# Kernel tuning notes

Measured on AMD Instinct MI355X. Metric: run time of the kernel, lower is better.

## Reference

```python
import jax, jax.numpy as jnp
import numpy as np

EPS = 1e-5
K = 5


def _bn(h, g, b):
    # BatchNorm1d in training mode: batch stats over all dims except channels.
    ax = tuple(range(h.ndim - 1))
    mu = jnp.mean(h, axis=ax, keepdims=True)
    var = jnp.var(h, axis=ax, keepdims=True)
    return g * (h - mu) * jax.lax.rsqrt(var + EPS) + b


def _block(x, w, b, g, be):
    # Lin -> ReLU -> BN, as in MLP() helper
    return _bn(jax.nn.relu(x @ w + b), g, be)


def _knn_idx(x, k):
    # x: [B, P, D]; k nearest per point (includes self at distance 0)
    sq = jnp.sum(x * x, axis=-1)
    d2 = sq[:, :, None] + sq[:, None, :] - 2.0 * jnp.einsum('bpd,bqd->bpq', x, x)
    return jax.lax.top_k(-d2, k)[1]  # [B, P, k]


def _edge_conv(x, k, mlp_fn):
    # DynamicEdgeConv: recompute kNN graph on current features, gather
    # neighbor/center pairs, per-edge MLP on [x_i, x_j - x_i], max-aggregate.
    idx = _knn_idx(x, k)                                   # [B,P,k]
    xj = jax.vmap(lambda xb, ib: xb[ib])(x, idx)           # [B,P,k,D]
    xi = jnp.broadcast_to(x[:, :, None, :], xj.shape)
    e = jnp.concatenate([xi, xj - xi], axis=-1)            # [B,P,k,2D]
    return jnp.max(mlp_fn(e), axis=2)                      # max aggr -> [B,P,C]


def dec_forward(pos,
                c1w0, c1b0, c1g0, c1e0,
                c1w1, c1b1, c1g1, c1e1,
                c1w2, c1b2, c1g2, c1e2,
                c2w, c2b, c2g, c2e,
                l1w, l1b, l1g, l1e,
                m1w, m1b, m1g, m1e,
                m2w, m2b, m2g, m2e,
                m3w, m3b):
    mlp1 = lambda e: _block(_block(_block(e, c1w0, c1b0, c1g0, c1e0),
                                   c1w1, c1b1, c1g1, c1e1),
                            c1w2, c1b2, c1g2, c1e2)
    x1 = _edge_conv(pos, K, mlp1)                          # [B,P,64]
    x2 = _edge_conv(x1, K, lambda e: _block(e, c2w, c2b, c2g, c2e))  # [B,P,128]
    h = _block(jnp.concatenate([x1, x2], axis=-1), l1w, l1b, l1g, l1e)  # [B,P,1024]
    p = jnp.max(h, axis=1)                                 # global_max_pool -> [B,1024]
    p = _block(p, m1w, m1b, m1g, m1e)                      # dropout omitted (eval)
    p = _block(p, m2w, m2b, m2g, m2e)
    return p @ m3w + m3b                                   # [B, n_classes]


def setup_inputs() -> dict:
    key = jax.random.key(0)
    ks = jax.random.split(key, 12)
    B, P = 16, 2048

    def w(k, shape):
        return 0.05 * jax.random.normal(k, shape, jnp.float32)

    z = lambda c: jnp.zeros((c,), jnp.float32)
    o = lambda c: jnp.ones((c,), jnp.float32)

    d = {
        'pos': jax.random.normal(ks[0], (B, P, 3), jnp.float32),
        'c1w0': w(ks[1], (6, 64)), 'c1b0': z(64), 'c1g0': o(64), 'c1e0': z(64),
        'c1w1': w(ks[2], (64, 64)), 'c1b1': z(64), 'c1g1': o(64), 'c1e1': z(64),
        'c1w2': w(ks[3], (64, 64)), 'c1b2': z(64), 'c1g2': o(64), 'c1e2': z(64),
        'c2w': w(ks[4], (128, 128)), 'c2b': z(128), 'c2g': o(128), 'c2e': z(128),
        'l1w': w(ks[5], (192, 1024)), 'l1b': z(1024), 'l1g': o(1024), 'l1e': z(1024),
        'm1w': w(ks[6], (1024, 512)), 'm1b': z(512), 'm1g': o(512), 'm1e': z(512),
        'm2w': w(ks[7], (512, 256)), 'm2b': z(256), 'm2g': o(256), 'm2e': z(256),
        'm3w': w(ks[8], (256, 2)), 'm3b': z(2),
    }
    return d


def reference(pos,
              c1w0, c1b0, c1g0, c1e0,
              c1w1, c1b1, c1g1, c1e1,
              c1w2, c1b2, c1g2, c1e2,
              c2w, c2b, c2g, c2e,
              l1w, l1b, l1g, l1e,
              m1w, m1b, m1g, m1e,
              m2w, m2b, m2g, m2e,
              m3w, m3b):
    return dec_forward(pos,
                       c1w0, c1b0, c1g0, c1e0,
                       c1w1, c1b1, c1g1, c1e1,
                       c1w2, c1b2, c1g2, c1e2,
                       c2w, c2b, c2g, c2e,
                       l1w, l1b, l1g, l1e,
                       m1w, m1b, m1g, m1e,
                       m2w, m2b, m2g, m2e,
                       m3w, m3b)
```

## Files before the change

### kernel.cpp

```cpp
#include <hip/hip_runtime.h>
#include <cmath>

constexpr int B = 16, P = 2048, KNN = 5;
constexpr int BP = B * P;
constexpr int E = BP * KNN;
constexpr float EPS = 1e-5f;
constexpr int QC2 = 2;

constexpr int ST0 = 0;
constexpr int ST1 = 128;
constexpr int ST2 = 256;
constexpr int ST3 = 384;
constexpr int ST4 = 640;
constexpr int ST5 = 2688;
constexpr int ST6 = 3712;
constexpr int ST_TOTAL = 4224;

typedef __attribute__((ext_vector_type(8))) short bf16x8;
typedef __attribute__((ext_vector_type(4))) float f32x4;

__device__ inline unsigned short f2bf(float x) {
    unsigned u = __float_as_uint(x);
    unsigned r = (u + 0x7FFFu + ((u >> 16) & 1u)) >> 16;
    return (unsigned short)r;
}
__device__ inline float bf2f(unsigned short h) {
    return __uint_as_float(((unsigned)h) << 16);
}
__device__ inline void split2bf(float x, unsigned short& h, unsigned short& l) {
    unsigned short hh = f2bf(x);
    h = hh;
    l = f2bf(x - bf2f(hh));
}

__device__ inline void ins5(float d, int qi, float bd[KNN], int bi[KNN]) {
    bool c0 = d < bd[0], c1 = d < bd[1], c2 = d < bd[2], c3 = d < bd[3], c4 = d < bd[4];
    bd[4] = c3 ? bd[3] : (c4 ? d : bd[4]);  bi[4] = c3 ? bi[3] : (c4 ? qi : bi[4]);
    bd[3] = c2 ? bd[2] : (c3 ? d : bd[3]);  bi[3] = c2 ? bi[2] : (c3 ? qi : bi[3]);
    bd[2] = c1 ? bd[1] : (c2 ? d : bd[2]);  bi[2] = c1 ? bi[1] : (c2 ? qi : bi[2]);
    bd[1] = c0 ? bd[0] : (c1 ? d : bd[1]);  bi[1] = c0 ? bi[0] : (c1 ? qi : bi[1]);
    bd[0] = c0 ? d : bd[0];                 bi[0] = c0 ? qi : bi[0];
}
__device__ inline void ins5t(float d, int qi, float bd[KNN], int bi[KNN]) {
    bool c0 = (d < bd[0]) || (d == bd[0] && qi < bi[0]);
    bool c1 = (d < bd[1]) || (d == bd[1] && qi < bi[1]);
    bool c2 = (d < bd[2]) || (d == bd[2] && qi < bi[2]);
    bool c3 = (d < bd[3]) || (d == bd[3] && qi < bi[3]);
    bool c4 = (d < bd[4]) || (d == bd[4] && qi < bi[4]);
    bd[4] = c3 ? bd[3] : (c4 ? d : bd[4]);  bi[4] = c3 ? bi[3] : (c4 ? qi : bi[4]);
    bd[3] = c2 ? bd[2] : (c3 ? d : bd[3]);  bi[3] = c2 ? bi[2] : (c3 ? qi : bi[3]);
    bd[2] = c1 ? bd[1] : (c2 ? d : bd[2]);  bi[2] = c1 ? bi[1] : (c2 ? qi : bi[2]);
    bd[1] = c0 ? bd[0] : (c1 ? d : bd[1]);  bi[1] = c0 ? bi[0] : (c1 ? qi : bi[1]);
    bd[0] = c0 ? d : bd[0];                 bi[0] = c0 ? qi : bi[0];
}

__global__ void k_init(float* __restrict__ stats, float* __restrict__ pmax,
                       float* __restrict__ pmin) {
    int i = blockIdx.x * 256 + threadIdx.x;
    if (i < ST_TOTAL) stats[i] = 0.f;
    if (i < B * 1024) { pmax[i] = 0.f; pmin[i] = INFINITY; }
}

__global__ __launch_bounds__(256) void k_redstat(const float* __restrict__ part,
        float* __restrict__ stats, int nblk) {
    __shared__ float r[256];
    int slot = blockIdx.x;
    float s = 0.f;
    for (int i = threadIdx.x; i < nblk; i += 256)
        s += part[(size_t)i * 128 + slot];
    r[threadIdx.x] = s; __syncthreads();
    for (int o = 128; o; o >>= 1) {
        if (threadIdx.x < o) r[threadIdx.x] += r[threadIdx.x + o];
        __syncthreads();
    }
    if (threadIdx.x == 0) stats[slot] = r[0];
}

__global__ void k_wsplit(const float* __restrict__ w, unsigned short* __restrict__ th,
                         unsigned short* __restrict__ tl, int K, int N) {
    int i = blockIdx.x * 256 + threadIdx.x;
    if (i >= K * N) return;
    int k = i / N, n = i - k * N;
    float f = w[i];
    unsigned short h = f2bf(f);
    th[(size_t)n * K + k] = h;
    tl[(size_t)n * K + k] = f2bf(f - bf2f(h));
}

__global__ __launch_bounds__(64) void k_wfold(const float* __restrict__ stats,
        const float* __restrict__ g, const float* __restrict__ be,
        const float* __restrict__ w, const float* __restrict__ bias,
        unsigned short* __restrict__ wfh, unsigned short* __restrict__ wfl,
        float* __restrict__ bias2, float invN) {
    __shared__ float red[64];
    int n = blockIdx.x, k = threadIdx.x;
    float mu = stats[k] * invN;
    float var = stats[64 + k] * invN - mu * mu;
    float sc = g[k] * rsqrtf(var + EPS);
    float sh = be[k] - mu * sc;
    float wv = w[k * 64 + n];
    float wf = sc * wv;
    unsigned short h, l;
    split2bf(wf, h, l);
    wfh[n * 64 + k] = h; wfl[n * 64 + k] = l;
    red[k] = sh * wv; __syncthreads();
    for (int o = 32; o; o >>= 1) {
        if (k < o) red[k] += red[k + o];
        __syncthreads();
    }
    if (k == 0) bias2[n] = bias[n] + red[0];
}

__global__ void k_wprep2(const float* __restrict__ w,
        unsigned short* __restrict__ wdh, unsigned short* __restrict__ wdl,
        unsigned short* __restrict__ w1h, unsigned short* __restrict__ w1l) {
    int i = blockIdx.x * 256 + threadIdx.x;
    if (i >= 64 * 128) return;
    int k = i >> 7, n = i & 127;
    float w0 = w[k * 128 + n];
    float w1 = w[(64 + k) * 128 + n];
    float wd = w0 - w1;
    unsigned short h, l;
    split2bf(wd, h, l); wdh[n * 64 + k] = h; wdl[n * 64 + k] = l;
    split2bf(w1, h, l); w1h[n * 64 + k] = h; w1l[n * 64 + k] = l;
}

__global__ void k_xsplit(const float* __restrict__ x, unsigned short* __restrict__ xh,
                         unsigned short* __restrict__ xl) {
    int i = blockIdx.x * 256 + threadIdx.x;
    float f = x[i];
    unsigned short h, l;
    split2bf(f, h, l);
    xh[i] = h; xl[i] = l;
}

__global__ __launch_bounds__(256) void k_knn1(const float* __restrict__ pos,
                                              int* __restrict__ idx1) {
    __shared__ float4 qt[2048];
    int b = blockIdx.x >> 5;
    int p0 = (blockIdx.x & 31) << 6;
    const float* posb = pos + (size_t)b * P * 3;
#pragma unroll
    for (int t = 0; t < 8; ++t) {
        int q = (t << 8) + threadIdx.x;
        float qx = posb[q * 3 + 0], qy = posb[q * 3 + 1], qz = posb[q * 3 + 2];
        qt[q] = make_float4(qx, qy, qz, qx * qx + qy * qy + qz * qz);
    }
    __syncthreads();
    int pl = threadIdx.x >> 2, sub = threadIdx.x & 3;
    int p = p0 + pl;
    float4 me = qt[p];
    float x = me.x, y = me.y, z = me.z, sqp = me.w;
    float bd[KNN]; int bi[KNN];
#pragma unroll
    for (int i = 0; i < KNN; ++i) { bd[i] = INFINITY; bi[i] = 0; }
    for (int j0 = 0; j0 < 512; j0 += 8) {
        float4 v[8];
#pragma unroll
        for (int u = 0; u < 8; ++u) v[u] = qt[((j0 + u) << 2) | sub];
#pragma unroll
        for (int u = 0; u < 8; ++u) {
            float dot = x * v[u].x + y * v[u].y + z * v[u].z;
            float d2 = sqp + v[u].w - 2.f * dot;
            if (d2 < bd[KNN - 1]) ins5(d2, ((j0 + u) << 2) | sub, bd, bi);
        }
    }
#pragma unroll
    for (int w = 1; w <= 2; w <<= 1) {
        float od[KNN]; int oi[KNN];
#pragma unroll
        for (int i = 0; i < KNN; ++i) {
            od[i] = __shfl_xor(bd[i], w, 64);
            oi[i] = __shfl_xor(bi[i], w, 64);
        }
#pragma unroll
        for (int i = 0; i < KNN; ++i) ins5t(od[i], oi[i], bd, bi);
    }
    if (sub == 0) {
        size_t o = ((size_t)b * P + p) * KNN;
#pragma unroll
        for (int i = 0; i < KNN; ++i) idx1[o + i] = bi[i];
    }
}

__global__ __launch_bounds__(256) void k_ec1_l0(const float* __restrict__ pos,
        const int* __restrict__ idx1, const float* __restrict__ w,
        const float* __restrict__ bias, unsigned short* __restrict__ zh,
        unsigned short* __restrict__ zl, float* __restrict__ part) {
    __shared__ float elds[256][6];
    __shared__ float red[256];
    int tid = threadIdx.x;
    int base = blockIdx.x * 256;
    {
        int e = base + tid;
        int bp = e / KNN;
        int bb = bp >> 11;
        int q = idx1[e];
        const float* pi = pos + (size_t)bp * 3;
        const float* pj = pos + ((size_t)(bb << 11) + q) * 3;
        float x0 = pi[0], x1v = pi[1], x2v = pi[2];
        elds[tid][0] = x0; elds[tid][1] = x1v; elds[tid][2] = x2v;
        elds[tid][3] = pj[0] - x0; elds[tid][4] = pj[1] - x1v; elds[tid][5] = pj[2] - x2v;
    }
    int c = tid & 63, lane = tid >> 6;
    float wr[6];
#pragma unroll
    for (int d = 0; d < 6; ++d) wr[d] = w[d * 64 + c];
    float bc = bias[c];
    __syncthreads();
    float s1 = 0.f, s2 = 0.f;
    for (int i = 0; i < 64; ++i) {
        int e = lane + (i << 2);
        float acc = bc;
#pragma unroll
        for (int d = 0; d < 6; ++d) acc = fmaf(elds[e][d], wr[d], acc);
        acc = fmaxf(acc, 0.f);
        unsigned short h, l;
        split2bf(acc, h, l);
        zh[(size_t)(base + e) * 64 + c] = h;
        zl[(size_t)(base + e) * 64 + c] = l;
        s1 += acc; s2 = fmaf(acc, acc, s2);
    }
    red[tid] = s1; __syncthreads();
    if (tid < 64) part[(size_t)blockIdx.x * 128 + tid] =
        red[tid] + red[tid + 64] + red[tid + 128] + red[tid + 192];
    __syncthreads();
    red[tid] = s2; __syncthreads();
    if (tid < 64) part[(size_t)blockIdx.x * 128 + 64 + tid] =
        red[tid] + red[tid + 64] + red[tid + 128] + red[tid + 192];
}

__global__ __launch_bounds__(128) void k_lin64m(
        const unsigned short* __restrict__ zinh, const unsigned short* __restrict__ zinl,
        const unsigned short* __restrict__ wfh, const unsigned short* __restrict__ wfl,
        const float* __restrict__ bias2, unsigned short* __restrict__ zouth,
        unsigned short* __restrict__ zoutl, float* __restrict__ part) {
    __shared__ float red[2 * 64 * 2];
    int tid = threadIdx.x;
    int wv = tid >> 6, lane = tid & 63;
    int l15 = lane & 15, quad = lane >> 4;
    int row0 = blockIdx.x * 128 + wv * 64;
    f32x4 acc[4][4];
#pragma unroll
    for (int i = 0; i < 4; ++i)
#pragma unroll
        for (int j = 0; j < 4; ++j) acc[i][j] = (f32x4)0.f;

#pragma unroll
    for (int kc = 0; kc < 2; ++kc) {
        bf16x8 afh[4], afl[4], bfh[4], bfl[4];
#pragma unroll
        for (int i = 0; i < 4; ++i) {
            size_t o = (size_t)(row0 + i * 16 + l15) * 64 + kc * 32 + quad * 8;
            afh[i] = *(const bf16x8*)&zinh[o];
            afl[i] = *(const bf16x8*)&zinl[o];
        }
#pragma unroll
        for (int j = 0; j < 4; ++j) {
            size_t wo = (size_t)(j * 16 + l15) * 64 + kc * 32 + quad * 8;
            bfh[j] = *(const bf16x8*)&wfh[wo];
            bfl[j] = *(const bf16x8*)&wfl[wo];
        }
#pragma unroll
        for (int i = 0; i < 4; ++i)
#pragma unroll
            for (int j = 0; j < 4; ++j) {
                acc[i][j] = __builtin_amdgcn_mfma_f32_16x16x32_bf16(afh[i], bfh[j], acc[i][j], 0, 0, 0);
                acc[i][j] = __builtin_amdgcn_mfma_f32_16x16x32_bf16(afh[i], bfl[j], acc[i][j], 0, 0, 0);
                acc[i][j] = __builtin_amdgcn_mfma_f32_16x16x32_bf16(afl[i], bfh[j], acc[i][j], 0, 0, 0);
            }
    }
#pragma unroll
    for (int j = 0; j < 4; ++j) {
        int colL = j * 16 + l15;
        float bl = bias2[colL];
        float s1 = 0.f, s2 = 0.f;
#pragma unroll
        for (int i = 0; i < 4; ++i) {
            int row = row0 + i * 16 + quad * 4;
#pragma unroll
            for (int r = 0; r < 4; ++r) {
                float v = fmaxf(acc[i][j][r] + bl, 0.f);
                unsigned short h, l;
                split2bf(v, h, l);
                zouth[(size_t)(row + r) * 64 + colL] = h;
                zoutl[(size_t)(row + r) * 64 + colL] = l;
                s1 += v; s2 = fmaf(v, v, s2);
            }
        }
        s1 += __shfl_xor(s1, 16, 64); s1 += __shfl_xor(s1, 32, 64);
        s2 += __shfl_xor(s2, 16, 64); s2 += __shfl_xor(s2, 32, 64);
        if (quad == 0) {
            red[(wv * 64 + colL) * 2 + 0] = s1;
            red[(wv * 64 + colL) * 2 + 1] = s2;
        }
    }
    __syncthreads();
    if (tid < 64) {
        part[(size_t)blockIdx.x * 128 + tid] =
            red[tid * 2] + red[(64 + tid) * 2];
        part[(size_t)blockIdx.x * 128 + 64 + tid] =
            red[tid * 2 + 1] + red[(64 + tid) * 2 + 1];
    }
}

__global__ __launch_bounds__(256) void k_ec1_fin(const unsigned short* __restrict__ z2h,
        const unsigned short* __restrict__ z2l,
        const float* __restrict__ statsIn, const float* __restrict__ g,
        const float* __restrict__ be, float* __restrict__ x1,
        float* __restrict__ sq2) {
    int tid = threadIdx.x;
    int o = blockIdx.x * 256 + tid;
    int c = o & 63; int bp = o >> 6;
    float mu = statsIn[c] * (1.f / E);
    float var = statsIn[64 + c] * (1.f / E) - mu * mu;
    float sc = g[c] * rsqrtf(var + EPS);
    float sh = be[c] - mu * sc;
    float m = -INFINITY;
#pragma unroll
    for (int j = 0; j < KNN; ++j) {
        size_t zo = ((size_t)bp * KNN + j) * 64 + c;
        float v = bf2f(z2h[zo]) + bf2f(z2l[zo]);
        m = fmaxf(m, fmaf(v, sc, sh));
    }
    x1[o] = m;
    float ss = m * m;
#pragma unroll
    for (int off = 32; off; off >>= 1) ss += __shfl_down(ss, off, 64);
    if (c == 0) sq2[bp] = ss;
}

__global__ __launch_bounds__(128, 1) void k_knn2(const unsigned short* __restrict__ x1h,
        const unsigned short* __restrict__ x1l, const float* __restrict__ sq2,
        float* __restrict__ cd, int* __restrict__ ci) {
    __shared__ float S[2][32 * 129];
    int tid = threadIdx.x;
    int wv = tid >> 6, lane = tid & 63;
    int l15 = lane & 15, quad = lane >> 4;
    int qc = blockIdx.x & (QC2 - 1);
    int pt = blockIdx.x >> 1;
    int b = pt >> 5;
    int pw = ((pt & 31) << 6) + wv * 32;
    const size_t xbase = (size_t)b * P * 64;
    float* Sw = &S[wv][0];

    bf16x8 ah[2][2], al[2][2];
#pragma unroll
    for (int i = 0; i < 2; ++i)
#pragma unroll
        for (int kc = 0; kc < 2; ++kc) {
            size_t o = xbase + (size_t)(pw + i * 16 + l15) * 64 + kc * 32 + quad * 8;
            ah[i][kc] = *(const bf16x8*)&x1h[o];
            al[i][kc] = *(const bf16x8*)&x1l[o];
        }

    int half = lane >> 5;
    int pidx = lane & 31;
    float bd[KNN]; int bi[KNN];
#pragma unroll
    for (int i = 0; i < KNN; ++i) { bd[i] = INFINITY; bi[i] = 0; }

    int qlo = qc << 10;
    for (int t = 0; t < 8; ++t) {
        int q0 = qlo + (t << 7);
        float qsv[8];
#pragma unroll
        for (int j = 0; j < 8; ++j) qsv[j] = sq2[b * P + q0 + j * 16 + l15];
        f32x4 acc[2][8];
#pragma unroll
        for (int i = 0; i < 2; ++i)
#pragma unroll
            for (int j = 0; j < 8; ++j) acc[i][j] = (f32x4)0.f;
#pragma unroll
        for (int kc = 0; kc < 2; ++kc) {
            bf16x8 bh[8], bl[8];
#pragma unroll
            for (int j = 0; j < 8; ++j) {
                size_t o = xbase + (size_t)(q0 + j * 16 + l15) * 64 + kc * 32 + quad * 8;
                bh[j] = *(const bf16x8*)&x1h[o];
                bl[j] = *(const bf16x8*)&x1l[o];
            }
#pragma unroll
            for (int i = 0; i < 2; ++i)
#pragma unroll
                for (int j = 0; j < 8; ++j) {
                    acc[i][j] = __builtin_amdgcn_mfma_f32_16x16x32_bf16(ah[i][kc], bh[j], acc[i][j], 0, 0, 0);
                    acc[i][j] = __builtin_amdgcn_mfma_f32_16x16x32_bf16(ah[i][kc], bl[j], acc[i][j], 0, 0, 0);
                    acc[i][j] = __builtin_amdgcn_mfma_f32_16x16x32_bf16(al[i][kc], bh[j], acc[i][j], 0, 0, 0);
                }
        }
#pragma unroll
        for (int i = 0; i < 2; ++i)
#pragma unroll
            for (int j = 0; j < 8; ++j)
#pragma unroll
                for (int r = 0; r < 4; ++r) {
                    int pl = i * 16 + quad * 4 + r;
                    Sw[pl * 129 + j * 16 + l15] = fmaf(acc[i][j][r], -2.f, qsv[j]);
                }
        const float* row = Sw + pidx * 129 + half * 64;
        int qb = q0 + half * 64;
        for (int jj = 0; jj < 64; jj += 4) {
            float k0 = row[jj + 0], k1 = row[jj + 1], k2 = row[jj + 2], k3 = row[jj + 3];
            if (k0 < bd[4]) ins5(k0, qb + jj + 0, bd, bi);
            if (k1 < bd[4]) ins5(k1, qb + jj + 1, bd, bi);
            if (k2 < bd[4]) ins5(k2, qb + jj + 2, bd, bi);
            if (k3 < bd[4]) ins5(k3, qb + jj + 3, bd, bi);
        }
    }
#pragma unroll
    for (int i = 0; i < KNN; ++i) {
        float od = __shfl_xor(bd[i], 32, 64);
        int oi = __shfl_xor(bi[i], 32, 64);
        if (half == 0) ins5t(od, oi, bd, bi);
    }
    if (half == 0) {
        size_t o = (((size_t)b * P + pw + pidx) * QC2 + qc) * KNN;
#pragma unroll
        for (int i = 0; i < KNN; ++i) { cd[o + i] = bd[i]; ci[o + i] = bi[i]; }
    }
}

__global__ __launch_bounds__(256) void k_knn2m(const float* __restrict__ cd,
        const int* __restrict__ ci, int* __restrict__ idx2) {
    int bp = blockIdx.x * 256 + threadIdx.x;
    float bd[KNN]; int bi[KNN];
#pragma unroll
    for (int i = 0; i < KNN; ++i) { bd[i] = INFINITY; bi[i] = 0; }
    size_t o = (size_t)bp * QC2 * KNN;
    for (int t = 0; t < QC2 * KNN; ++t) {
        float d2 = cd[o + t]; int qi = ci[o + t];
        if (d2 < bd[KNN - 1]) ins5(d2, qi, bd, bi);
    }
#pragma unroll
    for (int i = 0; i < KNN; ++i) idx2[bp * KNN + i] = bi[i];
}

__global__ __launch_bounds__(256) void k_ec2m(
        const unsigned short* __restrict__ x1h, const unsigned short* __restrict__ x1l,
        const int* __restrict__ idx2,
        const unsigned short* __restrict__ wdh, const unsigned short* __restrict__ wdl,
        const unsigned short* __restrict__ w1h, const unsigned short* __restrict__ w1l,
        const float* __restrict__ bias, float* __restrict__ zout,
        float* __restrict__ stats) {
    __shared__ float red[2 * 128 * 2];
    int tid = threadIdx.x;
    int base = blockIdx.x * 128;
    int bb = base / (P * KNN);
    int wv = tid >> 6, lane = tid & 63;
    int wm = wv >> 1, wn = wv & 1;
    int l15 = lane & 15, quad = lane >> 4;
    int rI[4], rJ[4];
#pragma unroll
    for (int i = 0; i < 4; ++i) {
        int e = base + wm * 64 + i * 16 + l15;
        rI[i] = e / KNN;
        rJ[i] = (bb << 11) + idx2[e];
    }
    f32x4 acc[4][4];
#pragma unroll
    for (int i = 0; i < 4; ++i)
#pragma unroll
        for (int j = 0; j < 4; ++j) acc[i][j] = (f32x4)0.f;

#pragma unroll
    for (int s = 0; s < 2; ++s) {
        const unsigned short* bh_ = s ? w1h : wdh;
        const unsigned short* bl_ = s ? w1l : wdl;
#pragma unroll
        for (int kc = 0; kc < 2; ++kc) {
            bf16x8 afh[4], afl[4], bfh[4], bfl[4];
#pragma unroll
            for (int i = 0; i < 4; ++i) {
                int row = s ? rJ[i] : rI[i];
                size_t o = (size_t)row * 64 + kc * 32 + quad * 8;
                afh[i] = *(const bf16x8*)&x1h[o];
                afl[i] = *(const bf16x8*)&x1l[o];
            }
#pragma unroll
            for (int j = 0; j < 4; ++j) {
                size_t wo = (size_t)(wn * 64 + j * 16 + l15) * 64 + kc * 32 + quad * 8;
                bfh[j] = *(const bf16x8*)&bh_[wo];
                bfl[j] = *(const bf16x8*)&bl_[wo];
            }
#pragma unroll
            for (int i = 0; i < 4; ++i)
#pragma unroll
                for (int j = 0; j < 4; ++j) {
                    acc[i][j] = __builtin_amdgcn_mfma_f32_16x16x32_bf16(afh[i], bfh[j], acc[i][j], 0, 0, 0);
                    acc[i][j] = __builtin_amdgcn_mfma_f32_16x16x32_bf16(afh[i], bfl[j], acc[i][j], 0, 0, 0);
                    acc[i][j] = __builtin_amdgcn_mfma_f32_16x16x32_bf16(afl[i], bfh[j], acc[i][j], 0, 0, 0);
                }
        }
    }
#pragma unroll
    for (int j = 0; j < 4; ++j) {
        int colL = wn * 64 + j * 16 + l15;
        float bl = bias[colL];
        float s1 = 0.f, s2 = 0.f;
#pragma unroll
        for (int i = 0; i < 4; ++i) {
            int row = wm * 64 + i * 16 + quad * 4;
#pragma unroll
            for (int r = 0; r < 4; ++r) {
                float v = fmaxf(acc[i][j][r] + bl, 0.f);
                zout[(size_t)(base + row + r) * 128 + colL] = v;
                s1 += v; s2 = fmaf(v, v, s2);
            }
        }
        s1 += __shfl_xor(s1, 16, 64); s1 += __shfl_xor(s1, 32, 64);
        s2 += __shfl_xor(s2, 16, 64); s2 += __shfl_xor(s2, 32, 64);
        if (quad == 0) {
            red[(wm * 128 + colL) * 2 + 0] = s1;
            red[(wm * 128 + colL) * 2 + 1] = s2;
        }
    }
    __syncthreads();
    if (tid < 128) {
        atomicAdd(&stats[tid], red[tid * 2] + red[(128 + tid) * 2]);
        atomicAdd(&stats[128 + tid], red[tid * 2 + 1] + red[(128 + tid) * 2 + 1]);
    }
}

__global__ __launch_bounds__(256) void k_ec2_fin(const float* __restrict__ z3,
        const float* __restrict__ stats, const float* __restrict__ g,
        const float* __restrict__ be, float* __restrict__ x2) {
    int o = blockIdx.x * 256 + threadIdx.x;
    int c = o & 127; int bp = o >> 7;
    float mu = stats[c] * (1.f / E);
    float var = stats[128 + c] * (1.f / E) - mu * mu;
    float sc = g[c] * rsqrtf(var + EPS);
    float sh = be[c] - mu * sc;
    float m = -INFINITY;
#pragma unroll
    for (int j = 0; j < KNN; ++j)
        m = fmaxf(m, fmaf(z3[((size_t)bp * KNN + j) * 128 + c], sc, sh));
    x2[o] = m;
}

__device__ __forceinline__ void gl16(unsigned short* lds, const unsigned short* g) {
    __builtin_amdgcn_global_load_lds(
        (const __attribute__((address_space(1))) unsigned int*)g,
        (__attribute__((address_space(3))) unsigned int*)lds, 16, 0, 0);
}

__global__ __launch_bounds__(256) void k_l1m(
        const unsigned short* __restrict__ x1h, const unsigned short* __restrict__ x1l,
        const unsigned short* __restrict__ x2h, const unsigned short* __restrict__ x2l,
        const unsigned short* __restrict__ wth, const unsigned short* __restrict__ wtl,
        const float* __restrict__ bias, float* __restrict__ stats,
        float* __restrict__ pmax, float* __restrict__ pmin) {
    __shared__ unsigned short Ah[128 * 32], Al[128 * 32];
    __shared__ unsigned short Bh[128 * 32], Bl[128 * 32];
    __shared__ float red[2 * 128 * 4];
    int tid = threadIdx.x;
    int brow = blockIdx.x & 255;
    int bcol = blockIdx.x >> 8;
    int row0 = brow << 7, col0 = bcol << 7;
    int wv = tid >> 6, lane = tid & 63;
    int wm = wv >> 1, wn = wv & 1;
    int l15 = lane & 15, quad = lane >> 4;
    int rloc = wv * 16 + (lane >> 2);
    int ch8 = (lane & 3) * 8;
    f32x4 acc[4][4];
#pragma unroll
    for (int i = 0; i < 4; ++i)
#pragma unroll
        for (int j = 0; j < 4; ++j) acc[i][j] = (f32x4)0.f;

#pragma unroll
    for (int t = 0; t < 6; ++t) {
        int k0 = t * 32;
        const unsigned short* ah = (k0 < 64) ? x1h : x2h;
        const unsigned short* al = (k0 < 64) ? x1l : x2l;
        int astr = (k0 < 64) ? 64 : 128;
        int aoff = (k0 < 64) ? k0 : (k0 - 64);
#pragma unroll
        for (int c = 0; c < 2; ++c) {
            int rl = c * 64 + rloc;
            size_t ao = (size_t)(row0 + rl) * astr + aoff + ch8;
            size_t bo = (size_t)(col0 + rl) * 192 + k0 + ch8;
            int lb = (c * 64 + wv * 16) * 32;
            gl16(&Ah[lb], &ah[ao]);
            gl16(&Al[lb], &al[ao]);
            gl16(&Bh[lb], &wth[bo]);
            gl16(&Bl[lb], &wtl[bo]);
        }
        __syncthreads();
        bf16x8 afh[4], afl[4], bfh[4], bfl[4];
#pragma unroll
        for (int i = 0; i < 4; ++i) {
            int o = (wm * 64 + i * 16 + l15) * 32 + quad * 8;
            afh[i] = *(const bf16x8*)&Ah[o];
            afl[i] = *(const bf16x8*)&Al[o];
        }
#pragma unroll
        for (int j = 0; j < 4; ++j) {
            int o = (wn * 64 + j * 16 + l15) * 32 + quad * 8;
            bfh[j] = *(const bf16x8*)&Bh[o];
            bfl[j] = *(const bf16x8*)&Bl[o];
        }
#pragma unroll
        for (int i = 0; i < 4; ++i)
#pragma unroll
            for (int j = 0; j < 4; ++j) {
                acc[i][j] = __builtin_amdgcn_mfma_f32_16x16x32_bf16(afh[i], bfh[j], acc[i][j], 0, 0, 0);
                acc[i][j] = __builtin_amdgcn_mfma_f32_16x16x32_bf16(afh[i], bfl[j], acc[i][j], 0, 0, 0);
                acc[i][j] = __builtin_amdgcn_mfma_f32_16x16x32_bf16(afl[i], bfh[j], acc[i][j], 0, 0, 0);
            }
        __syncthreads();
    }
#pragma unroll
    for (int j = 0; j < 4; ++j) {
        int colL = wn * 64 + j * 16 + l15;
        float bl = bias[col0 + colL];
        float s1 = 0.f, s2 = 0.f, mx = 0.f, mn = INFINITY;
#pragma unroll
        for (int i = 0; i < 4; ++i)
#pragma unroll
            for (int r = 0; r < 4; ++r) {
                float v = fmaxf(acc[i][j][r] + bl, 0.f);
                s1 += v; s2 = fmaf(v, v, s2);
                mx = fmaxf(mx, v); mn = fminf(mn, v);
            }
        s1 += __shfl_xor(s1, 16, 64); s1 += __shfl_xor(s1, 32, 64);
        s2 += __shfl_xor(s2, 16, 64); s2 += __shfl_xor(s2, 32, 64);
        mx = fmaxf(mx, __shfl_xor(mx, 16, 64)); mx = fmaxf(mx, __shfl_xor(mx, 32, 64));
        mn = fminf(mn, __shfl_xor(mn, 16, 64)); mn = fminf(mn, __shfl_xor(mn, 32, 64));
        if (quad == 0) {
            float* rp = &red[(wm * 128 + colL) * 4];
            rp[0] = s1; rp[1] = s2; rp[2] = mx; rp[3] = mn;
        }
    }
    __syncthreads();
    if (tid < 128) {
        const float* r0 = &red[tid * 4];
        const float* r1 = &red[(128 + tid) * 4];
        int bb = row0 >> 11;
        atomicAdd(&stats[col0 + tid], r0[0] + r1[0]);
        atomicAdd(&stats[1024 + col0 + tid], r0[1] + r1[1]);
        atomicMax((unsigned int*)&pmax[bb * 1024 + col0 + tid],
                  __float_as_uint(fmaxf(r0[2], r1[2])));
        atomicMin((unsigned int*)&pmin[bb * 1024 + col0 + tid],
                  __float_as_uint(fminf(r0[3], r1[3])));
    }
}

__global__ void k_pool(const float* __restrict__ stats, const float* __restrict__ g,
                       const float* __restrict__ be, const float* __restrict__ pmax,
                       const float* __restrict__ pmin, float* __restrict__ p) {
    int o = blockIdx.x * 256 + threadIdx.x;
    int c = o & 1023;
    float mu = stats[c] * (1.f / BP);
    float var = stats[1024 + c] * (1.f / BP) - mu * mu;
    float sc = g[c] * rsqrtf(var + EPS);
    float sh = be[c] - mu * sc;
    float v = (sc >= 0.f) ? pmax[o] : pmin[o];
    p[o] = fmaf(v, sc, sh);
}

__global__ __launch_bounds__(256) void k_m1(const float* __restrict__ p,
        const float* __restrict__ w, const float* __restrict__ bias,
        float* __restrict__ t1, float* __restrict__ stats) {
    int o = blockIdx.x * 256 + threadIdx.x;
    int c = o & 511, b = o >> 9;
    const float* pr = p + (b << 10);
    float acc = bias[c];
    for (int k = 0; k < 1024; ++k) acc = fmaf(pr[k], w[k * 512 + c], acc);
    acc = fmaxf(acc, 0.f);
    t1[o] = acc;
    atomicAdd(&stats[c], acc);
    atomicAdd(&stats[512 + c], acc * acc);
}

__global__ __launch_bounds__(256) void k_m2(const float* __restrict__ t1,
        const float* __restrict__ stats5, const float* __restrict__ g,
        const float* __restrict__ be, const float* __restrict__ w,
        const float* __restrict__ bias, float* __restrict__ t2,
        float* __restrict__ stats6) {
    __shared__ float scl[512], shf[512];
    int tid = threadIdx.x;
    for (int t = tid; t < 512; t += 256) {
        float mu = stats5[t] * (1.f / 16.f);
        float var = stats5[512 + t] * (1.f / 16.f) - mu * mu;
        float sc = g[t] * rsqrtf(var + EPS);
        scl[t] = sc; shf[t] = be[t] - mu * sc;
    }
    __syncthreads();
    int o = blockIdx.x * 256 + tid;
    int c = o & 255, b = o >> 8;
    const float* tr = t1 + (b << 9);
    float acc = bias[c];
    for (int k = 0; k < 512; ++k) {
        float u = fmaf(tr[k], scl[k], shf[k]);
        acc = fmaf(u, w[k * 256 + c], acc);
    }
    acc = fmaxf(acc, 0.f);
    t2[o] = acc;
    atomicAdd(&stats6[c], acc);
    atomicAdd(&stats6[256 + c], acc * acc);
}

__global__ __launch_bounds__(256) void k_m3(const float* __restrict__ t2,
        const float* __restrict__ stats6, const float* __restrict__ g,
        const float* __restrict__ be, const float* __restrict__ w,
        const float* __restrict__ bias, float* __restrict__ out) {
    __shared__ float scl[256], shf[256];
    int tid = threadIdx.x;
    {
        float mu = stats6[tid] * (1.f / 16.f);
        float var = stats6[256 + tid] * (1.f / 16.f) - mu * mu;
        float sc = g[tid] * rsqrtf(var + EPS);
        scl[tid] = sc; shf[tid] = be[tid] - mu * sc;
    }
    __syncthreads();
    if (tid < 32) {
        int c = tid & 1, b = tid >> 1;
        const float* tr = t2 + (b << 8);
        float acc = bias[c];
        for (int k = 0; k < 256; ++k) {
            float u = fmaf(tr[k], scl[k], shf[k]);
            acc = fmaf(u, w[k * 2 + c], acc);
        }
        out[tid] = acc;
    }
}

extern "C" void kernel_launch(void* const* d_in, const int* in_sizes, int n_in,
                              void* d_out, int out_size, void* d_ws, size_t ws_size,
                              hipStream_t stream) {
    const float* pos  = (const float*)d_in[0];
    const float* c1w0 = (const float*)d_in[1];
    const float* c1b0 = (const float*)d_in[2];
    const float* c1g0 = (const float*)d_in[3];
    const float* c1e0 = (const float*)d_in[4];
    const float* c1w1 = (const float*)d_in[5];
    const float* c1b1 = (const float*)d_in[6];
    const float* c1g1 = (const float*)d_in[7];
    const float* c1e1 = (const float*)d_in[8];
    const float* c1w2 = (const float*)d_in[9];
    const float* c1b2 = (const float*)d_in[10];
    const float* c1g2 = (const float*)d_in[11];
    const float* c1e2 = (const float*)d_in[12];
    const float* c2w  = (const float*)d_in[13];
    const float* c2b  = (const float*)d_in[14];
    const float* c2g  = (const float*)d_in[15];
    const float* c2e  = (const float*)d_in[16];
    const float* l1w  = (const float*)d_in[17];
    const float* l1b  = (const float*)d_in[18];
    const float* l1g  = (const float*)d_in[19];
    const float* l1e  = (const float*)d_in[20];
    const float* m1w  = (const float*)d_in[21];
    const float* m1b  = (const float*)d_in[22];
    const float* m1g  = (const float*)d_in[23];
    const float* m1e  = (const float*)d_in[24];
    const float* m2w  = (const float*)d_in[25];
    const float* m2b  = (const float*)d_in[26];
    const float* m2g  = (const float*)d_in[27];
    const float* m2e  = (const float*)d_in[28];
    const float* m3w  = (const float*)d_in[29];
    const float* m3b  = (const float*)d_in[30];
    float* out = (float*)d_out;

    char* ws = (char*)d_ws;
    size_t off = 0;
    auto alloc = [&](size_t bytes) {
        size_t r = off; off = (off + bytes + 255) & ~(size_t)255; return r;
    };
    float* stats = (float*)(ws + alloc(ST_TOTAL * 4));
    float* pmax  = (float*)(ws + alloc(16 * 1024 * 4));
    float* pmin  = (float*)(ws + alloc(16 * 1024 * 4));
    float* pbuf  = (float*)(ws + alloc(16 * 1024 * 4));
    float* t1    = (float*)(ws + alloc(16 * 512 * 4));
    float* t2    = (float*)(ws + alloc(16 * 256 * 4));
    float* sq2   = (float*)(ws + alloc((size_t)BP * 4));
    float* part  = (float*)(ws + alloc((size_t)(E / 64) * 128 * 4));
    unsigned short* wthL = (unsigned short*)(ws + alloc((size_t)192 * 1024 * 2));
    unsigned short* wtlL = (unsigned short*)(ws + alloc((size_t)192 * 1024 * 2));
    unsigned short* wdh  = (unsigned short*)(ws + alloc((size_t)128 * 64 * 2));
    unsigned short* wdl  = (unsigned short*)(ws + alloc((size_t)128 * 64 * 2));
    unsigned short* w1h  = (unsigned short*)(ws + alloc((size_t)128 * 64 * 2));
    unsigned short* w1l  = (unsigned short*)(ws + alloc((size_t)128 * 64 * 2));
    unsigned short* wf1h = (unsigned short*)(ws + alloc((size_t)64 * 64 * 2));
    unsigned short* wf1l = (unsigned short*)(ws + alloc((size_t)64 * 64 * 2));
    unsigned short* wf2h = (unsigned short*)(ws + alloc((size_t)64 * 64 * 2));
    unsigned short* wf2l = (unsigned short*)(ws + alloc((size_t)64 * 64 * 2));
    float* bias2a = (float*)(ws + alloc(64 * 4));
    float* bias2b = (float*)(ws + alloc(64 * 4));
    int*   idx1  = (int*)  (ws + alloc((size_t)E * 4));
    int*   idx2  = (int*)  (ws + alloc((size_t)E * 4));
    float* x1    = (float*)(ws + alloc((size_t)BP * 64 * 4));
    float* x2    = (float*)(ws + alloc((size_t)BP * 128 * 4));
    float* zA    = (float*)(ws + alloc((size_t)E * 128 * 4));
    float* zB    = (float*)(ws + alloc((size_t)E * 64 * 4));
    unsigned short* z0h = (unsigned short*)zA;
    unsigned short* z0l = z0h + (size_t)E * 64;
    unsigned short* z1h = z0l + (size_t)E * 64;
    unsigned short* z1l = z1h + (size_t)E * 64;
    unsigned short* z2h = (unsigned short*)zB;
    unsigned short* z2l = z2h + (size_t)E * 64;
    unsigned short* x1h = (unsigned short*)zB;
    unsigned short* x1l = x1h + (size_t)BP * 64;
    float* cand_d = (float*)(x1l + (size_t)BP * 64);
    int*   cand_i = (int*)(cand_d + (size_t)BP * QC2 * KNN);
    unsigned short* x2h = (unsigned short*)(cand_i + (size_t)BP * QC2 * KNN);
    unsigned short* x2l = x2h + (size_t)BP * 128;

    (void)in_sizes; (void)n_in; (void)out_size; (void)ws_size;

    k_init<<<64, 256, 0, stream>>>(stats, pmax, pmin);
    k_wsplit<<<(192 * 1024 + 255) / 256, 256, 0, stream>>>(l1w, wthL, wtlL, 192, 1024);
    k_wprep2<<<(64 * 128 + 255) / 256, 256, 0, stream>>>(c2w, wdh, wdl, w1h, w1l);
    k_knn1<<<B * 32, 256, 0, stream>>>(pos, idx1);
    k_ec1_l0<<<E / 256, 256, 0, stream>>>(pos, idx1, c1w0, c1b0, z0h, z0l, part);
    k_redstat<<<128, 256, 0, stream>>>(part, stats + ST0, E / 256);
    k_wfold<<<64, 64, 0, stream>>>(stats + ST0, c1g0, c1e0, c1w1, c1b1,
                                   wf1h, wf1l, bias2a, 1.f / E);
    k_lin64m<<<E / 128, 128, 0, stream>>>(z0h, z0l, wf1h, wf1l, bias2a,
                                          z1h, z1l, part);
    k_redstat<<<128, 256, 0, stream>>>(part, stats + ST1, E / 128);
    k_wfold<<<64, 64, 0, stream>>>(stats + ST1, c1g1, c1e1, c1w2, c1b2,
                                   wf2h, wf2l, bias2b, 1.f / E);
    k_lin64m<<<E / 128, 128, 0, stream>>>(z1h, z1l, wf2h, wf2l, bias2b,
                                          z2h, z2l, part);
    k_redstat<<<128, 256, 0, stream>>>(part, stats + ST2, E / 128);
    k_ec1_fin<<<BP * 64 / 256, 256, 0, stream>>>(z2h, z2l, stats + ST2, c1g2, c1e2,
                                                 x1, sq2);
    k_xsplit<<<BP * 64 / 256, 256, 0, stream>>>(x1, x1h, x1l);
    k_knn2<<<B * 32 * QC2, 128, 0, stream>>>(x1h, x1l, sq2, cand_d, cand_i);
    k_knn2m<<<BP / 256, 256, 0, stream>>>(cand_d, cand_i, idx2);
    k_ec2m<<<E / 128, 256, 0, stream>>>(x1h, x1l, idx2, wdh, wdl, w1h, w1l,
                                        c2b, zA, stats + ST3);
    k_ec2_fin<<<BP * 128 / 256, 256, 0, stream>>>(zA, stats + ST3, c2g, c2e, x2);
    k_xsplit<<<BP * 128 / 256, 256, 0, stream>>>(x2, x2h, x2l);
    k_l1m<<<256 * 8, 256, 0, stream>>>(x1h, x1l, x2h, x2l, wthL, wtlL, l1b,
                                       stats + ST4, pmax, pmin);
    k_pool<<<64, 256, 0, stream>>>(stats + ST4, l1g, l1e, pmax, pmin, pbuf);
    k_m1<<<32, 256, 0, stream>>>(pbuf, m1w, m1b, t1, stats + ST5);
    k_m2<<<16, 256, 0, stream>>>(t1, stats + ST5, m1g, m1e, m2w, m2b, t2, stats + ST6);
    k_m3<<<1, 256, 0, stream>>>(t2, stats + ST6, m2g, m2e, m3w, m3b, out);
}
```

Baseline: 586.6 us.

## Keep kNN2 top-k in registers via transposed MFMA and shuffle merges

The second kNN kernel now computes the distance tile transposed, so each lane holds distances for its own points. It inserts them directly into per-lane top-5 lists in registers, then merges the lists across lanes with xor shuffles. This removes the shared-memory staging of the distance tile. The query range is split into four chunks instead of two and occupancy is raised to 3 blocks per CU to expose more parallelism. In exchange, every candidate now goes through an unconditional branchless insertion, and register pressure rises.

```diff
diff --git a/kernel.cpp b/kernel.cpp
--- a/kernel.cpp
+++ b/kernel.cpp
@@ -5,7 +5,9 @@
 constexpr int BP = B * P;
 constexpr int E = BP * KNN;
 constexpr float EPS = 1e-5f;
-constexpr int QC2 = 2;
+constexpr int QC2 = 4;
+constexpr int QC2_SHIFT = 2;
+static_assert(QC2 == (1 << QC2_SHIFT), "QC2 pow2");
 
 constexpr int ST0 = 0;
 constexpr int ST1 = 128;
@@ -52,6 +54,16 @@
     bd[2] = c1 ? bd[1] : (c2 ? d : bd[2]);  bi[2] = c1 ? bi[1] : (c2 ? qi : bi[2]);
     bd[1] = c0 ? bd[0] : (c1 ? d : bd[1]);  bi[1] = c0 ? bi[0] : (c1 ? qi : bi[1]);
     bd[0] = c0 ? d : bd[0];                 bi[0] = c0 ? qi : bi[0];
+}
+__device__ inline void merge_xor(int w, float bd[KNN], int bi[KNN]) {
+    float od[KNN]; int oi[KNN];
+#pragma unroll
+    for (int k = 0; k < KNN; ++k) {
+        od[k] = __shfl_xor(bd[k], w, 64);
+        oi[k] = __shfl_xor(bi[k], w, 64);
+    }
+#pragma unroll
+    for (int k = 0; k < KNN; ++k) ins5t(od[k], oi[k], bd, bi);
 }
 
 __global__ void k_init(float* __restrict__ stats, float* __restrict__ pmax,
@@ -330,94 +342,91 @@
     if (c == 0) sq2[bp] = ss;
 }
 
-__global__ __launch_bounds__(128, 1) void k_knn2(const unsigned short* __restrict__ x1h,
+__global__ __launch_bounds__(128, 3) void k_knn2(const unsigned short* __restrict__ x1h,
         const unsigned short* __restrict__ x1l, const float* __restrict__ sq2,
         float* __restrict__ cd, int* __restrict__ ci) {
-    __shared__ float S[2][32 * 129];
     int tid = threadIdx.x;
     int wv = tid >> 6, lane = tid & 63;
     int l15 = lane & 15, quad = lane >> 4;
     int qc = blockIdx.x & (QC2 - 1);
-    int pt = blockIdx.x >> 1;
+    int pt = blockIdx.x >> QC2_SHIFT;
     int b = pt >> 5;
     int pw = ((pt & 31) << 6) + wv * 32;
     const size_t xbase = (size_t)b * P * 64;
-    float* Sw = &S[wv][0];
-
-    bf16x8 ah[2][2], al[2][2];
+
+    bf16x8 ph[2][2], pl_[2][2];
 #pragma unroll
     for (int i = 0; i < 2; ++i)
 #pragma unroll
         for (int kc = 0; kc < 2; ++kc) {
             size_t o = xbase + (size_t)(pw + i * 16 + l15) * 64 + kc * 32 + quad * 8;
-            ah[i][kc] = *(const bf16x8*)&x1h[o];
-            al[i][kc] = *(const bf16x8*)&x1l[o];
-        }
-
-    int half = lane >> 5;
-    int pidx = lane & 31;
-    float bd[KNN]; int bi[KNN];
-#pragma unroll
-    for (int i = 0; i < KNN; ++i) { bd[i] = INFINITY; bi[i] = 0; }
-
-    int qlo = qc << 10;
-    for (int t = 0; t < 8; ++t) {
+            ph[i][kc] = *(const bf16x8*)&x1h[o];
+            pl_[i][kc] = *(const bf16x8*)&x1l[o];
+        }
+
+    float bd0[KNN], bd1[KNN]; int bi0[KNN], bi1[KNN];
+#pragma unroll
+    for (int i = 0; i < KNN; ++i) {
+        bd0[i] = INFINITY; bi0[i] = 0;
+        bd1[i] = INFINITY; bi1[i] = 0;
+    }
+
+    int qlo = qc * (P / QC2);
+#pragma unroll
+    for (int t = 0; t < (P / QC2) / 128; ++t) {
         int q0 = qlo + (t << 7);
         float qsv[8];
 #pragma unroll
         for (int j = 0; j < 8; ++j) qsv[j] = sq2[b * P + q0 + j * 16 + l15];
-        f32x4 acc[2][8];
-#pragma unroll
-        for (int i = 0; i < 2; ++i)
-#pragma unroll
-            for (int j = 0; j < 8; ++j) acc[i][j] = (f32x4)0.f;
-#pragma unroll
-        for (int kc = 0; kc < 2; ++kc) {
-            bf16x8 bh[8], bl[8];
-#pragma unroll
-            for (int j = 0; j < 8; ++j) {
-                size_t o = xbase + (size_t)(q0 + j * 16 + l15) * 64 + kc * 32 + quad * 8;
-                bh[j] = *(const bf16x8*)&x1h[o];
-                bl[j] = *(const bf16x8*)&x1l[o];
+#pragma unroll
+        for (int jg = 0; jg < 2; ++jg) {
+            f32x4 acc[4][2];
+#pragma unroll
+            for (int u = 0; u < 4; ++u)
+#pragma unroll
+                for (int i = 0; i < 2; ++i) acc[u][i] = (f32x4)0.f;
+#pragma unroll
+            for (int kc = 0; kc < 2; ++kc) {
+                bf16x8 qh[4], ql_[4];
+#pragma unroll
+                for (int u = 0; u < 4; ++u) {
+                    int j = jg * 4 + u;
+                    size_t o = xbase + (size_t)(q0 + j * 16 + l15) * 64 + kc * 32 + quad * 8;
+                    qh[u] = *(const bf16x8*)&x1h[o];
+                    ql_[u] = *(const bf16x8*)&x1l[o];
+                }
+#pragma unroll
+                for (int u = 0; u < 4; ++u)
+#pragma unroll
+                    for (int i = 0; i < 2; ++i) {
+                        acc[u][i] = __builtin_amdgcn_mfma_f32_16x16x32_bf16(qh[u], ph[i][kc], acc[u][i], 0, 0, 0);
+                        acc[u][i] = __builtin_amdgcn_mfma_f32_16x16x32_bf16(qh[u], pl_[i][kc], acc[u][i], 0, 0, 0);
+                        acc[u][i] = __builtin_amdgcn_mfma_f32_16x16x32_bf16(ql_[u], ph[i][kc], acc[u][i], 0, 0, 0);
+                    }
             }
 #pragma unroll
-            for (int i = 0; i < 2; ++i)
-#pragma unroll
-                for (int j = 0; j < 8; ++j) {
-                    acc[i][j] = __builtin_amdgcn_mfma_f32_16x16x32_bf16(ah[i][kc], bh[j], acc[i][j], 0, 0, 0);
-                    acc[i][j] = __builtin_amdgcn_mfma_f32_16x16x32_bf16(ah[i][kc], bl[j], acc[i][j], 0, 0, 0);
-                    acc[i][j] = __builtin_amdgcn_mfma_f32_16x16x32_bf16(al[i][kc], bh[j], acc[i][j], 0, 0, 0);
+            for (int u = 0; u < 4; ++u) {
+                int j = jg * 4 + u;
+#pragma unroll
+                for (int r = 0; r < 4; ++r) {
+                    float sqq = __shfl(qsv[j], (quad << 2) + r, 16);
+                    int qi = q0 + j * 16 + (quad << 2) + r;
+                    ins5(fmaf(acc[u][0][r], -2.f, sqq), qi, bd0, bi0);
+                    ins5(fmaf(acc[u][1][r], -2.f, sqq), qi, bd1, bi1);
                 }
-        }
-#pragma unroll
-        for (int i = 0; i < 2; ++i)
-#pragma unroll
-            for (int j = 0; j < 8; ++j)
-#pragma unroll
-                for (int r = 0; r < 4; ++r) {
-                    int pl = i * 16 + quad * 4 + r;
-                    Sw[pl * 129 + j * 16 + l15] = fmaf(acc[i][j][r], -2.f, qsv[j]);
-                }
-        const float* row = Sw + pidx * 129 + half * 64;
-        int qb = q0 + half * 64;
-        for (int jj = 0; jj < 64; jj += 4) {
-            float k0 = row[jj + 0], k1 = row[jj + 1], k2 = row[jj + 2], k3 = row[jj + 3];
-            if (k0 < bd[4]) ins5(k0, qb + jj + 0, bd, bi);
-            if (k1 < bd[4]) ins5(k1, qb + jj + 1, bd, bi);
-            if (k2 < bd[4]) ins5(k2, qb + jj + 2, bd, bi);
-            if (k3 < bd[4]) ins5(k3, qb + jj + 3, bd, bi);
-        }
-    }
-#pragma unroll
-    for (int i = 0; i < KNN; ++i) {
-        float od = __shfl_xor(bd[i], 32, 64);
-        int oi = __shfl_xor(bi[i], 32, 64);
-        if (half == 0) ins5t(od, oi, bd, bi);
-    }
-    if (half == 0) {
-        size_t o = (((size_t)b * P + pw + pidx) * QC2 + qc) * KNN;
-#pragma unroll
-        for (int i = 0; i < KNN; ++i) { cd[o + i] = bd[i]; ci[o + i] = bi[i]; }
+            }
+        }
+    }
+    merge_xor(16, bd0, bi0); merge_xor(16, bd1, bi1);
+    merge_xor(32, bd0, bi0); merge_xor(32, bd1, bi1);
+    if (quad == 0) {
+        size_t o0 = (((size_t)b * P + pw + l15) * QC2 + qc) * KNN;
+        size_t o1 = (((size_t)b * P + pw + 16 + l15) * QC2 + qc) * KNN;
+#pragma unroll
+        for (int k = 0; k < KNN; ++k) {
+            cd[o0 + k] = bd0[k]; ci[o0 + k] = bi0[k];
+            cd[o1 + k] = bd1[k]; ci[o1 + k] = bi1[k];
+        }
     }
 }
 
```

Result: slower. 1.133 ms (+93.1%).
